# Performance work log

Hardware: AMD Instinct MI355X
Metric: run time of the kernel (lower is better)

## Reference

```python
import jax, jax.numpy as jnp
import numpy as np
import math

DIM = 1024
NH = 16
HD = DIM // NH
SEQ = 2048
B = 2
P = 16
HIDDEN = 2816  # multiple_of*ceil(int(2*4*dim/3)/multiple_of)


def justnorm(x, axis=-1):
    n = jnp.sqrt(jnp.sum(x * x, axis=axis, keepdims=True))
    return x / jnp.maximum(n, 1e-12)


def adafm_modulate(x, ftime, p):
    # x: [B,H,W]; ftime: [B, p*p] real
    Bb, H, W = x.shape
    xp = x.reshape(Bb, H // p, p, W // p, p).transpose(0, 1, 3, 2, 4).reshape(Bb, H // p, W // p, p * p)
    fspec = jnp.fft.fft2(xp)  # over last two axes (W//p, p*p)
    fspec = fspec * ftime.reshape(Bb, 1, 1, p * p)
    fout = jnp.fft.ifft2(fspec).real
    fout = fout.reshape(Bb, H // p, W // p, p, p).transpose(0, 1, 3, 2, 4).reshape(Bb, H, W)
    return fout


def apply_rotary(xq, xk, cos, sin):
    # xq,xk: [B,S,NH,HD]; cos,sin: [S, HD//2]
    def rot(t):
        tr = t.reshape(*t.shape[:-1], HD // 2, 2)
        a, b = tr[..., 0], tr[..., 1]
        c = cos[None, :, None, :]
        s = sin[None, :, None, :]
        ra = a * c - b * s
        rb = a * s + b * c
        return jnp.stack([ra, rb], axis=-1).reshape(t.shape)
    return rot(xq), rot(xk)


def attention(x, cos, sin, wq, wk, wv, wo, sqk):
    bsz, seqlen, _ = x.shape
    xq = (x @ wq).reshape(bsz, seqlen, NH, HD)
    xk = (x @ wk).reshape(bsz, seqlen, NH, HD)
    xv = (x @ wv).reshape(bsz, seqlen, NH, HD)
    xq, xk = apply_rotary(xq, xk, cos, sin)
    sqk_eff = (sqk * math.sqrt(DIM)).reshape(1, 1, NH, HD)  # sqk_init_value/sqk_init_scaling = sqrt(dim)
    xq = sqk_eff * justnorm(xq)
    xk = sqk_eff * justnorm(xk)
    scale = HD ** 0.5
    scores = jnp.einsum('bqhd,bkhd->bhqk', xq, xk) * scale
    attn = jax.nn.softmax(scores, axis=-1)
    out = jnp.einsum('bhqk,bkhd->bqhd', attn, xv).reshape(bsz, seqlen, DIM)
    return out @ wo


def feed_forward(x, w1, w2, w3, su, sv):
    x1 = x @ w1
    x3 = x @ w3
    scale = math.sqrt(HIDDEN)
    h = jax.nn.silu(x1 * sv * scale) * (x3 * su)
    return h @ w2


def setup_inputs() -> dict:
    key = jax.random.key(0)
    ks = jax.random.split(key, 12)
    inv = 1.0 / (10000.0 ** (np.arange(0, HD, 2, dtype=np.float32) / HD))
    ang = np.outer(np.arange(SEQ, dtype=np.float32), inv)
    s = 0.02
    return {
        'x': jax.random.normal(ks[0], (B, SEQ, DIM), jnp.float32),
        'freqs_cos': jnp.asarray(np.cos(ang), jnp.float32),
        'freqs_sin': jnp.asarray(np.sin(ang), jnp.float32),
        'adafm_input': jax.random.normal(ks[1], (B, DIM), jnp.float32),
        'wq': jax.random.normal(ks[2], (DIM, DIM), jnp.float32) * s,
        'wk': jax.random.normal(ks[3], (DIM, DIM), jnp.float32) * s,
        'wv': jax.random.normal(ks[4], (DIM, DIM), jnp.float32) * s,
        'wo': jax.random.normal(ks[5], (DIM, DIM), jnp.float32) * s,
        'sqk': jnp.full((DIM,), 1.0 / math.sqrt(DIM), jnp.float32),
        'w1': jax.random.normal(ks[6], (DIM, HIDDEN), jnp.float32) * s,
        'w2': jax.random.normal(ks[7], (HIDDEN, DIM), jnp.float32) * s,
        'w3': jax.random.normal(ks[8], (DIM, HIDDEN), jnp.float32) * s,
        'su': jnp.ones((HIDDEN,), jnp.float32),
        'sv': jnp.ones((HIDDEN,), jnp.float32),
        'proj_w': jax.random.normal(ks[9], (DIM, 2 * P * P), jnp.float32) * s,
        'proj_b': jnp.zeros((2 * P * P,), jnp.float32),
        'attn_alpha': jnp.full((DIM,), 0.05 / math.sqrt(DIM), jnp.float32),
        'mlp_alpha': jnp.full((DIM,), 0.05 / math.sqrt(DIM), jnp.float32),
    }


def reference(x, freqs_cos, freqs_sin, adafm_input, wq, wk, wv, wo, sqk, w1, w2, w3, su, sv, proj_w, proj_b, attn_alpha, mlp_alpha):
    # AdaFM projection: SiLU -> Linear
    t = jax.nn.silu(adafm_input) @ proj_w + proj_b  # [B, 2*P*P]
    msa_time, mlp_time = t[:, :P * P], t[:, P * P:]

    alpha_scale = 0.05 * math.sqrt(DIM)  # attn_alpha_init_value / attn_alpha_init_scaling
    lr = jnp.abs(attn_alpha * alpha_scale)
    h = justnorm(x)
    h_a = attention(adafm_modulate(x, msa_time, P), freqs_cos, freqs_sin, wq, wk, wv, wo, sqk)
    h_a = justnorm(h_a)
    x = justnorm(h + lr * (h_a - h))

    lr = jnp.abs(mlp_alpha * alpha_scale)
    h = justnorm(x)
    h_m = feed_forward(adafm_modulate(x, mlp_time, P), w1, w2, w3, su, sv)
    h_m = justnorm(h_m)
    x = justnorm(h + lr * (h_m - h))
    return x
```

## Files before the change

### kernel.cpp

```cpp
#include <hip/hip_runtime.h>
#include <hip/hip_bf16.h>
#include <math.h>

#define SEQ    2048
#define DIMN   1024
#define NHEAD  16
#define HDIM   64
#define BATCH  2
#define ROWS   4096
#define HIDDEN 2816
#define FCHUNK 2048
#define QKVS   3072

typedef __attribute__((ext_vector_type(8))) short short8;
typedef __attribute__((ext_vector_type(4))) float f32x4;
typedef unsigned short ushort_t;
typedef __attribute__((address_space(1))) void gas_t;
typedef __attribute__((address_space(3))) void las_t;

__device__ __forceinline__ float bfbits(ushort_t u){ return __uint_as_float(((unsigned)u) << 16); }
__device__ __forceinline__ ushort_t f2bu(float f){
  __hip_bfloat16 h = __float2bfloat16(f);
  return *reinterpret_cast<ushort_t*>(&h);
}
__device__ __forceinline__ ushort_t f2bu_t(float f){ return (ushort_t)(__float_as_uint(f) >> 16); }
__device__ __forceinline__ float ldv(const float* p){ return *p; }
__device__ __forceinline__ float ldv(const ushort_t* p){ return bfbits(*p); }
__device__ __forceinline__ void stv(float* p, float v){ *p = v; }
__device__ __forceinline__ void stv(ushort_t* p, float v){ *p = f2bu(v); }
__device__ __forceinline__ void async_cp16(const ushort_t* g, ushort_t* l){
  __builtin_amdgcn_global_load_lds((gas_t*)g, (las_t*)l, 16, 0, 0);
}
__device__ __forceinline__ ushort4 ld4u(const float* p){
  float4 v = *(const float4*)p;
  ushort4 u; u.x = f2bu(v.x); u.y = f2bu(v.y); u.z = f2bu(v.z); u.w = f2bu(v.w);
  return u;
}
__device__ __forceinline__ ushort4 ld4u(const ushort_t* p){ return *(const ushort4*)p; }

__global__ void k_time(const float* __restrict__ ada, const float* __restrict__ pw,
                       const float* __restrict__ pb, float* __restrict__ t){
  int b = blockIdx.x >> 9, o = blockIdx.x & 511, lane = threadIdx.x;
  float acc = 0.f;
  for(int i = lane; i < DIMN; i += 64){
    float a = ada[b*DIMN + i];
    float s = a / (1.f + expf(-a));
    acc += s * pw[i*512 + o];
  }
  for(int off = 32; off; off >>= 1) acc += __shfl_down(acc, off);
  if(lane == 0) t[b*512 + o] = acc + pb[o];
}

__global__ void k_gp(const float* __restrict__ t, ushort_t* __restrict__ Gpk){
  __shared__ float gl[256];
  int wb = blockIdx.x, kc = blockIdx.y, tid = threadIdx.x;
  int b = wb & 1, which = wb >> 1;
  const float C = 6.283185307179586f / 256.f;
  float acc = 0.f;
  for(int k = 0; k < 256; k++){
    float f = t[b*512 + which*256 + k];
    acc += f * cosf(C * (float)((k*tid) & 255));
  }
  gl[tid] = acc * (1.f/256.f);
  __syncthreads();
  ushort_t* ob = Gpk + ((size_t)(wb*8 + kc))*8192;
  for(int rep = 0; rep < 4; rep++){
    int n = rep*64 + (tid >> 2), mmb = (tid & 3)*8;
    short8 o;
    #pragma unroll
    for(int j = 0; j < 8; j++)
      o[j] = (short)f2bu(gl[(n - kc*32 - (mmb + j)) & 255]);
    *(short8*)(ob + n*32 + mmb) = o;
  }
}

#define APAD 264
#define GPAD 40
template<typename IN>
__global__ __launch_bounds__(256) void k_modmf(const IN* __restrict__ src,
        const ushort_t* __restrict__ Gpk, ushort_t* __restrict__ dst){
  __shared__ __align__(16) ushort_t Ap[64*APAD];
  __shared__ __align__(16) ushort_t Gs[128*GPAD];
  int nh = blockIdx.x, i = blockIdx.y, b = blockIdx.z;
  int tid = threadIdx.x, lane = tid & 63, w = tid >> 6;
  int l15 = lane & 15, quad = lane >> 4;
  const IN* xb = src + (size_t)b*SEQ*DIMN + (size_t)(i*16)*DIMN;
  int j = tid >> 2, c = (tid & 3)*4;
  #pragma unroll 4
  for(int rep = 0; rep < 16; rep++){
    ushort4 v4 = ld4u(xb + (size_t)rep*DIMN + tid*4);
    *(ushort4*)&Ap[j*APAD + rep*16 + c] = v4;
  }
  f32x4 acc[8];
  #pragma unroll
  for(int nt = 0; nt < 8; nt++){ acc[nt][0]=0.f; acc[nt][1]=0.f; acc[nt][2]=0.f; acc[nt][3]=0.f; }
  for(int kc = 0; kc < 8; kc++){
    __syncthreads();
    {
      const ushort_t* gsrc = Gpk + ((size_t)(b*8 + kc))*8192 + nh*4096;
      #pragma unroll
      for(int r2 = 0; r2 < 2; r2++){
        int n = r2*64 + (tid >> 2), mm = (tid & 3)*8;
        *(short8*)&Gs[n*GPAD + mm] = *(const short8*)(gsrc + r2*2048 + tid*8);
      }
    }
    __syncthreads();
    short8 af = *(const short8*)&Ap[(w*16 + l15)*APAD + kc*32 + quad*8];
    #pragma unroll
    for(int nt = 0; nt < 8; nt++){
      short8 bf = *(const short8*)&Gs[(nt*16 + l15)*GPAD + quad*8];
      acc[nt] = __builtin_amdgcn_mfma_f32_16x16x32_bf16(af, bf, acc[nt], 0, 0, 0);
    }
  }
  size_t ob = (size_t)b*SEQ*DIMN + (size_t)(i*16 + nh*8)*DIMN + (w*16 + quad*4)*16 + l15;
  #pragma unroll
  for(int nt = 0; nt < 8; nt++)
    #pragma unroll
    for(int t = 0; t < 4; t++)
      dst[ob + (size_t)nt*DIMN + t*16] = f2bu(acc[nt][t]);
}

__global__ void k_wt(const float* __restrict__ W, ushort_t* __restrict__ Wt, int K, int N){
  __shared__ float tile[32][33];
  int k0 = blockIdx.y*32, n0 = blockIdx.x*32;
  int r = threadIdx.x >> 3, c4 = (threadIdx.x & 7)*4;
  float4 v = *(const float4*)(W + (size_t)(k0 + r)*N + n0 + c4);
  tile[r][c4+0] = v.x; tile[r][c4+1] = v.y; tile[r][c4+2] = v.z; tile[r][c4+3] = v.w;
  __syncthreads();
  ushort4 o;
  o.x = f2bu(tile[c4+0][r]); o.y = f2bu(tile[c4+1][r]);
  o.z = f2bu(tile[c4+2][r]); o.w = f2bu(tile[c4+3][r]);
  *(ushort4*)(Wt + (size_t)(n0 + r)*K + k0 + c4) = o;
}

template<int BM, int BN, typename OUT>
__global__ __launch_bounds__(256) void k_gemm_mf(const ushort_t* __restrict__ A,
        const ushort_t* __restrict__ Wt, OUT* __restrict__ C, int N, int K){
  constexpr int MT = BM/32, NT = BN/32;
  constexpr int AI = BM/64, BI = BN/64;
  __shared__ __align__(16) ushort_t As[BM*32];
  __shared__ __align__(16) ushort_t Bs[BN*32];
  int tid = threadIdx.x, lane = tid & 63, w = tid >> 6;
  int l15 = lane & 15, quad = lane >> 4;
  int m0 = blockIdx.y*BM, n0 = blockIdx.x*BN;
  int wr = (w>>1)*(BM/2), wc = (w&1)*(BN/2);
  int srow = lane >> 2, scol = (lane & 3)*8;
  const ushort_t* ag[AI]; ushort_t* al[AI];
  const ushort_t* bg[BI]; ushort_t* bl[BI];
  #pragma unroll
  for(int i = 0; i < AI; i++){
    int rb = w*AI + i;
    ag[i] = A + (size_t)(m0 + rb*16 + srow)*K + scol;
    al[i] = As + rb*512 + lane*8;
  }
  #pragma unroll
  for(int i = 0; i < BI; i++){
    int rb = w*BI + i;
    bg[i] = Wt + (size_t)(n0 + rb*16 + srow)*K + scol;
    bl[i] = Bs + rb*512 + lane*8;
  }
  f32x4 acc[MT][NT];
  #pragma unroll
  for(int mt = 0; mt < MT; mt++)
    #pragma unroll
    for(int nt = 0; nt < NT; nt++)
      for(int t = 0; t < 4; t++) acc[mt][nt][t] = 0.f;
  for(int kk = 0; kk < K; kk += 32){
    __syncthreads();
    #pragma unroll
    for(int i = 0; i < AI; i++) async_cp16(ag[i] + kk, al[i]);
    #pragma unroll
    for(int i = 0; i < BI; i++) async_cp16(bg[i] + kk, bl[i]);
    __syncthreads();
    short8 af[MT], bf[NT];
    #pragma unroll
    for(int mt = 0; mt < MT; mt++) af[mt] = *(const short8*)&As[(wr + mt*16 + l15)*32 + quad*8];
    #pragma unroll
    for(int nt = 0; nt < NT; nt++) bf[nt] = *(const short8*)&Bs[(wc + nt*16 + l15)*32 + quad*8];
    #pragma unroll
    for(int mt = 0; mt < MT; mt++)
      #pragma unroll
      for(int nt = 0; nt < NT; nt++)
        acc[mt][nt] = __builtin_amdgcn_mfma_f32_16x16x32_bf16(af[mt], bf[nt], acc[mt][nt], 0, 0, 0);
  }
  #pragma unroll
  for(int mt = 0; mt < MT; mt++)
    #pragma unroll
    for(int nt = 0; nt < NT; nt++)
      #pragma unroll
      for(int t = 0; t < 4; t++)
        stv(C + (size_t)(m0 + wr + mt*16 + quad*4 + t)*N + n0 + wc + nt*16 + l15, acc[mt][nt][t]);
}

__global__ __launch_bounds__(256) void k_ffn12(const ushort_t* __restrict__ A,
        const ushort_t* __restrict__ W1t, const ushort_t* __restrict__ W3t,
        const float* __restrict__ su, const float* __restrict__ sv,
        ushort_t* __restrict__ H, int K){
  __shared__ __align__(16) ushort_t As[128*32];
  __shared__ __align__(16) ushort_t B1s[64*32];
  __shared__ __align__(16) ushort_t B3s[64*32];
  int tid = threadIdx.x, lane = tid & 63, w = tid >> 6;
  int l15 = lane & 15, quad = lane >> 4;
  int m0 = blockIdx.y*128, n0 = blockIdx.x*64;
  int wr = (w>>1)*64, wc = (w&1)*32;
  int srow = lane >> 2, scol = (lane & 3)*8;
  const ushort_t* ag[2]; ushort_t* al[2];
  #pragma unroll
  for(int i = 0; i < 2; i++){
    int rb = w*2 + i;
    ag[i] = A + (size_t)(m0 + rb*16 + srow)*K + scol;
    al[i] = As + rb*512 + lane*8;
  }
  const ushort_t* b1g = W1t + (size_t)(n0 + w*16 + srow)*K + scol;
  const ushort_t* b3g = W3t + (size_t)(n0 + w*16 + srow)*K + scol;
  ushort_t* b1l = B1s + w*512 + lane*8;
  ushort_t* b3l = B3s + w*512 + lane*8;
  f32x4 acc1[4][2], acc3[4][2];
  #pragma unroll
  for(int mt = 0; mt < 4; mt++)
    #pragma unroll
    for(int nt = 0; nt < 2; nt++)
      for(int t = 0; t < 4; t++){ acc1[mt][nt][t] = 0.f; acc3[mt][nt][t] = 0.f; }
  for(int kk = 0; kk < K; kk += 32){
    __syncthreads();
    async_cp16(ag[0] + kk, al[0]);
    async_cp16(ag[1] + kk, al[1]);
    async_cp16(b1g + kk, b1l);
    async_cp16(b3g + kk, b3l);
    __syncthreads();
    short8 af[4], b1f[2], b3f[2];
    #pragma unroll
    for(int mt = 0; mt < 4; mt++) af[mt] = *(const short8*)&As[(wr + mt*16 + l15)*32 + quad*8];
    #pragma unroll
    for(int nt = 0; nt < 2; nt++){
      b1f[nt] = *(const short8*)&B1s[(wc + nt*16 + l15)*32 + quad*8];
      b3f[nt] = *(const short8*)&B3s[(wc + nt*16 + l15)*32 + quad*8];
    }
    #pragma unroll
    for(int mt = 0; mt < 4; mt++)
      #pragma unroll
      for(int nt = 0; nt < 2; nt++){
        acc1[mt][nt] = __builtin_amdgcn_mfma_f32_16x16x32_bf16(af[mt], b1f[nt], acc1[mt][nt], 0, 0, 0);
        acc3[mt][nt] = __builtin_amdgcn_mfma_f32_16x16x32_bf16(af[mt], b3f[nt], acc3[mt][nt], 0, 0, 0);
      }
  }
  #pragma unroll
  for(int nt = 0; nt < 2; nt++){
    int n = n0 + wc + nt*16 + l15;
    float svv = sv[n] * 53.06599665f, suv = su[n];
    #pragma unroll
    for(int mt = 0; mt < 4; mt++)
      #pragma unroll
      for(int t = 0; t < 4; t++){
        float hpre = acc1[mt][nt][t] * svv;
        float sil = hpre / (1.f + expf(-hpre));
        float hv = sil * (acc3[mt][nt][t] * suv);
        H[(size_t)(m0 + wr + mt*16 + quad*4 + t)*HIDDEN + n] = f2bu(hv);
      }
  }
}

__global__ void k_qkvprep(ushort_t* __restrict__ qkv, const float* __restrict__ fc,
        const float* __restrict__ fs, const float* __restrict__ sqk){
  int w = threadIdx.x >> 6, d = threadIdx.x & 63;
  int h = blockIdx.x*4 + w, s = blockIdx.y, b = blockIdx.z;
  size_t ib = ((size_t)(b*SEQ + s))*QKVS + h*HDIM + d;
  float q = bfbits(qkv[ib]), k = bfbits(qkv[ib + 1024]);
  float qn = __shfl_xor(q, 1), kn = __shfl_xor(k, 1);
  int p = d >> 1;
  float c = fc[s*32 + p], sn = fs[s*32 + p];
  float qr, kr;
  if((d & 1) == 0){ qr = q*c - qn*sn; kr = k*c - kn*sn; }
  else            { qr = qn*sn + q*c; kr = kn*sn + k*c; }
  float sq = qr*qr, sk = kr*kr;
  for(int off = 32; off; off >>= 1){ sq += __shfl_xor(sq, off); sk += __shfl_xor(sk, off); }
  float scl = sqk[h*HDIM + d] * 32.f;
  qkv[ib]        = f2bu(scl * qr / fmaxf(sqrtf(sq), 1e-12f));
  qkv[ib + 1024] = f2bu(scl * kr / fmaxf(sqrtf(sk), 1e-12f));
}

__global__ void k_vt(const ushort_t* __restrict__ qkv, ushort_t* __restrict__ vto){
  __shared__ ushort_t tile[64][72];
  int s0 = blockIdx.x*64, h = blockIdx.y, b = blockIdx.z;
  int r = threadIdx.x >> 2, c = (threadIdx.x & 3)*16;
  const ushort_t* src = qkv + (size_t)(b*SEQ + s0 + r)*QKVS + 2048 + h*HDIM + c;
  *(short8*)&tile[r][c]     = *(const short8*)src;
  *(short8*)&tile[r][c + 8] = *(const short8*)(src + 8);
  __syncthreads();
  ushort_t* dst = vto + ((size_t)(b*NHEAD + h)*HDIM + r)*SEQ + s0 + c;
  for(int j = 0; j < 16; j += 4){
    ushort4 o;
    o.x = tile[c+j][r]; o.y = tile[c+j+1][r]; o.z = tile[c+j+2][r]; o.w = tile[c+j+3][r];
    *(ushort4*)(dst + j) = o;
  }
}

#define LSTR 72
__global__ __launch_bounds__(256) void k_flash_mf(const ushort_t* __restrict__ qkv,
        const ushort_t* __restrict__ vt, ushort_t* __restrict__ out){
  int qb = blockIdx.x, h = blockIdx.y, b = blockIdx.z;
  int tid = threadIdx.x, lane = tid & 63, w = tid >> 6;
  int l15 = lane & 15, quad = lane >> 4;
  __shared__ __align__(16) ushort_t Ks[64*LSTR], Vts[64*LSTR];
  __shared__ __align__(16) ushort_t Ps[4][32*LSTR];
  size_t qkb = (size_t)b*SEQ*QKVS + h*HDIM;
  const ushort_t* vb = vt + (size_t)(b*NHEAD + h)*HDIM*SEQ;
  short8 qf[2][2];
  #pragma unroll
  for(int qm = 0; qm < 2; qm++){
    const ushort_t* qrow = qkv + qkb + (size_t)(qb*128 + w*32 + qm*16 + l15)*QKVS;
    qf[qm][0] = *(const short8*)(qrow + quad*8);
    qf[qm][1] = *(const short8*)(qrow + 32 + quad*8);
  }
  f32x4 o_acc[2][4];
  #pragma unroll
  for(int qm = 0; qm < 2; qm++)
    #pragma unroll
    for(int g = 0; g < 4; g++){ o_acc[qm][g][0]=0.f; o_acc[qm][g][1]=0.f; o_acc[qm][g][2]=0.f; o_acc[qm][g][3]=0.f; }
  float lsum[2] = {0.f, 0.f};
  int sr = tid >> 2, sc = tid & 3;
  const float C1 = 11.54156036f;
  const float C2 = 11.90223409f;
  for(int ch = 0; ch < SEQ/64; ch++){
    __syncthreads();
    {
      const ushort_t* krow = qkv + qkb + (size_t)(b ? 0 : 0) + (size_t)(ch*64 + sr)*QKVS + 1024 + sc*16;
      short8 k0 = *(const short8*)krow, k1 = *(const short8*)(krow + 8);
      const ushort_t* vrow = vb + (size_t)sr*SEQ + ch*64 + sc*16;
      short8 v0 = *(const short8*)vrow, v1 = *(const short8*)(vrow + 8);
      *(short8*)&Ks[sr*LSTR + sc*16]      = k0;
      *(short8*)&Ks[sr*LSTR + sc*16 + 8]  = k1;
      *(short8*)&Vts[sr*LSTR + sc*16]     = v0;
      *(short8*)&Vts[sr*LSTR + sc*16 + 8] = v1;
    }
    __syncthreads();
    #pragma unroll
    for(int g = 0; g < 4; g++){
      short8 k0 = *(const short8*)&Ks[(g*16 + l15)*LSTR + quad*8];
      short8 k1 = *(const short8*)&Ks[(g*16 + l15)*LSTR + 32 + quad*8];
      #pragma unroll
      for(int qm = 0; qm < 2; qm++){
        f32x4 sa; sa[0]=0.f; sa[1]=0.f; sa[2]=0.f; sa[3]=0.f;
        sa = __builtin_amdgcn_mfma_f32_16x16x32_bf16(k0, qf[qm][0], sa, 0, 0, 0);
        sa = __builtin_amdgcn_mfma_f32_16x16x32_bf16(k1, qf[qm][1], sa, 0, 0, 0);
        float e0 = exp2f(fmaf(sa[0], C1, -C2));
        float e1 = exp2f(fmaf(sa[1], C1, -C2));
        float e2 = exp2f(fmaf(sa[2], C1, -C2));
        float e3 = exp2f(fmaf(sa[3], C1, -C2));
        lsum[qm] += (e0 + e1) + (e2 + e3);
        ushort4 pk;
        pk.x = f2bu_t(e0); pk.y = f2bu_t(e1); pk.z = f2bu_t(e2); pk.w = f2bu_t(e3);
        *(ushort4*)&Ps[w][(qm*16 + l15)*LSTR + g*16 + quad*4] = pk;
      }
    }
    __syncthreads();
    short8 a[2][2];
    #pragma unroll
    for(int qm = 0; qm < 2; qm++){
      a[qm][0] = *(const short8*)&Ps[w][(qm*16 + l15)*LSTR + quad*8];
      a[qm][1] = *(const short8*)&Ps[w][(qm*16 + l15)*LSTR + 32 + quad*8];
    }
    #pragma unroll
    for(int g = 0; g < 4; g++){
      short8 b0 = *(const short8*)&Vts[(g*16 + l15)*LSTR + quad*8];
      short8 b1 = *(const short8*)&Vts[(g*16 + l15)*LSTR + 32 + quad*8];
      #pragma unroll
      for(int qm = 0; qm < 2; qm++){
        o_acc[qm][g] = __builtin_amdgcn_mfma_f32_16x16x32_bf16(a[qm][0], b0, o_acc[qm][g], 0, 0, 0);
        o_acc[qm][g] = __builtin_amdgcn_mfma_f32_16x16x32_bf16(a[qm][1], b1, o_acc[qm][g], 0, 0, 0);
      }
    }
  }
  #pragma unroll
  for(int qm = 0; qm < 2; qm++){
    float ls = lsum[qm];
    ls += __shfl_xor(ls, 16);
    ls += __shfl_xor(ls, 32);
    #pragma unroll
    for(int t = 0; t < 4; t++){
      float inv = 1.f / __shfl(ls, quad*4 + t);
      #pragma unroll
      for(int g = 0; g < 4; g++)
        out[(size_t)b*SEQ*DIMN + (size_t)(qb*128 + w*32 + qm*16 + quad*4 + t)*DIMN + h*HDIM + g*16 + l15]
          = f2bu(o_acc[qm][g][t] * inv);
    }
  }
}

__device__ __forceinline__ float blockReduceSum(float v, float* red){
  for(int off = 32; off; off >>= 1) v += __shfl_xor(v, off);
  int wid = threadIdx.x >> 6;
  if((threadIdx.x & 63) == 0) red[wid] = v;
  __syncthreads();
  float tot = red[0] + red[1] + red[2] + red[3];
  __syncthreads();
  return tot;
}

template<typename T1, typename T2, typename TO>
__global__ void k_rn(const T1* __restrict__ x, const T2* __restrict__ ha,
        const float* __restrict__ alpha, TO* __restrict__ xo){
  __shared__ float red[4];
  int row = blockIdx.x, tid = threadIdx.x;
  size_t base = (size_t)row * DIMN;
  float xs[4], hs[4], cs[4];
  float s1 = 0.f, s2 = 0.f;
  for(int j = 0; j < 4; j++){
    int i = tid + j*256;
    float xv = ldv(x + base + i);  xs[j] = xv; s1 += xv*xv;
    float hv = ldv(ha + base + i); hs[j] = hv; s2 += hv*hv;
  }
  s1 = blockReduceSum(s1, red);
  s2 = blockReduceSum(s2, red);
  float r1 = 1.f / fmaxf(sqrtf(s1), 1e-12f);
  float r2 = 1.f / fmaxf(sqrtf(s2), 1e-12f);
  float s3 = 0.f;
  for(int j = 0; j < 4; j++){
    int i = tid + j*256;
    float lr = fabsf(alpha[i] * 1.6f);
    float hn = xs[j] * r1;
    float cv = hn + lr*(hs[j]*r2 - hn);
    cs[j] = cv; s3 += cv*cv;
  }
  s3 = blockReduceSum(s3, red);
  float r3 = 1.f / fmaxf(sqrtf(s3), 1e-12f);
  for(int j = 0; j < 4; j++){
    int i = tid + j*256;
    stv(xo + base + i, cs[j] * r3);
  }
}

extern "C" void kernel_launch(void* const* d_in, const int* in_sizes, int n_in,
                              void* d_out, int out_size, void* d_ws, size_t ws_size,
                              hipStream_t stream){
  const float* x   = (const float*)d_in[0];
  const float* fc  = (const float*)d_in[1];
  const float* fs  = (const float*)d_in[2];
  const float* ada = (const float*)d_in[3];
  const float* wq  = (const float*)d_in[4];
  const float* wk  = (const float*)d_in[5];
  const float* wv  = (const float*)d_in[6];
  const float* wo  = (const float*)d_in[7];
  const float* sqk = (const float*)d_in[8];
  const float* w1  = (const float*)d_in[9];
  const float* w2  = (const float*)d_in[10];
  const float* w3  = (const float*)d_in[11];
  const float* su  = (const float*)d_in[12];
  const float* sv  = (const float*)d_in[13];
  const float* pw  = (const float*)d_in[14];
  const float* pb  = (const float*)d_in[15];
  const float* aal = (const float*)d_in[16];
  const float* mal = (const float*)d_in[17];
  float* out = (float*)d_out;

  const size_t MM = (size_t)DIMN*DIMN;
  const size_t HM = (size_t)HIDDEN*DIMN;
  const size_t F  = (size_t)ROWS*DIMN;
  char* wsb = (char*)d_ws;
  float* t = (float*)wsb;
  ushort_t* Gpk = (ushort_t*)(wsb + 16384);
  ushort_t* wqT = Gpk + 262144;
  ushort_t* wkT = wqT + MM;
  ushort_t* wvT = wkT + MM;
  ushort_t* woT = wvT + MM;
  ushort_t* w1T = woT + MM;
  ushort_t* w3T = w1T + HM;
  ushort_t* w2T = w3T + HM;
  ushort_t* P1  = w2T + HM;
  ushort_t* QKV = P1 + F;
  ushort_t* Ha  = QKV;
  ushort_t* M2  = QKV + F;
  ushort_t* Hm  = QKV + 2*F;
  ushort_t* a1  = QKV + 3*F;
  ushort_t* Vt  = a1;

  dim3 blk(256);

  k_time<<<dim3(1024), dim3(64), 0, stream>>>(ada, pw, pb, t);
  k_gp<<<dim3(4,8), blk, 0, stream>>>(t, Gpk);

  k_wt<<<dim3(32,32), blk, 0, stream>>>(wq, wqT, DIMN, DIMN);
  k_wt<<<dim3(32,32), blk, 0, stream>>>(wk, wkT, DIMN, DIMN);
  k_wt<<<dim3(32,32), blk, 0, stream>>>(wv, wvT, DIMN, DIMN);
  k_wt<<<dim3(32,32), blk, 0, stream>>>(wo, woT, DIMN, DIMN);
  k_wt<<<dim3(HIDDEN/32,32), blk, 0, stream>>>(w1, w1T, DIMN, HIDDEN);
  k_wt<<<dim3(HIDDEN/32,32), blk, 0, stream>>>(w3, w3T, DIMN, HIDDEN);
  k_wt<<<dim3(32,HIDDEN/32), blk, 0, stream>>>(w2, w2T, HIDDEN, DIMN);

  k_modmf<float><<<dim3(2,128,BATCH), blk, 0, stream>>>(x, Gpk, P1);
  k_gemm_mf<128,128,ushort_t><<<dim3(24,32), blk, 0, stream>>>(P1, wqT, QKV, QKVS, DIMN);
  k_qkvprep<<<dim3(NHEAD/4,SEQ,BATCH), blk, 0, stream>>>(QKV, fc, fs, sqk);
  k_vt<<<dim3(SEQ/64,NHEAD,BATCH), blk, 0, stream>>>(QKV, Vt);
  k_flash_mf<<<dim3(SEQ/128,NHEAD,BATCH), blk, 0, stream>>>(QKV, Vt, P1);
  k_gemm_mf<128,128,ushort_t><<<dim3(8,32), blk, 0, stream>>>(P1, woT, Ha, DIMN, DIMN);
  k_rn<float,ushort_t,ushort_t><<<dim3(ROWS), blk, 0, stream>>>(x, Ha, aal, P1);

  k_modmf<ushort_t><<<dim3(2,128,BATCH), blk, 0, stream>>>(P1, Gpk + 131072, M2);
  for(int c2 = 0; c2 < ROWS/FCHUNK; c2++){
    const ushort_t* Ac = M2 + (size_t)c2*FCHUNK*DIMN;
    k_ffn12<<<dim3(HIDDEN/64,FCHUNK/128), blk, 0, stream>>>(Ac, w1T, w3T, su, sv, a1, DIMN);
    k_gemm_mf<128,128,ushort_t><<<dim3(8,FCHUNK/128), blk, 0, stream>>>(a1, w2T, Hm + (size_t)c2*FCHUNK*DIMN, DIMN, HIDDEN);
  }

  k_rn<ushort_t,ushort_t,float><<<dim3(ROWS), blk, 0, stream>>>(P1, Hm, mal, out);
}
```

Measured before the change: 578.5 us.

## Halve flash query tile, prefetch K/V into registers, shrink output GEMM tiles

The flash attention kernel now handles 64 queries per block (16 per wave) instead of 128. This doubles the grid and cuts registers and LDS per block. K/V tiles for the next chunk are loaded into registers while the current chunk is computed, and the barrier between writing and reading P is dropped because each wave only touches its own P slice. The wo and w2 GEMM launches switch to smaller tiles so more blocks fill the GPU, at the cost of less reuse per block and more redundant K/V loads across blocks.

After: 512.4 us. 11.4% less time.

```diff
diff --git a/kernel.cpp b/kernel.cpp
--- a/kernel.cpp
+++ b/kernel.cpp
@@ -302,88 +302,74 @@
   int tid = threadIdx.x, lane = tid & 63, w = tid >> 6;
   int l15 = lane & 15, quad = lane >> 4;
   __shared__ __align__(16) ushort_t Ks[64*LSTR], Vts[64*LSTR];
-  __shared__ __align__(16) ushort_t Ps[4][32*LSTR];
+  __shared__ __align__(16) ushort_t Ps[4][16*LSTR];
   size_t qkb = (size_t)b*SEQ*QKVS + h*HDIM;
+  size_t ob  = (size_t)b*SEQ*DIMN + h*HDIM;
   const ushort_t* vb = vt + (size_t)(b*NHEAD + h)*HDIM*SEQ;
-  short8 qf[2][2];
-  #pragma unroll
-  for(int qm = 0; qm < 2; qm++){
-    const ushort_t* qrow = qkv + qkb + (size_t)(qb*128 + w*32 + qm*16 + l15)*QKVS;
-    qf[qm][0] = *(const short8*)(qrow + quad*8);
-    qf[qm][1] = *(const short8*)(qrow + 32 + quad*8);
-  }
-  f32x4 o_acc[2][4];
-  #pragma unroll
-  for(int qm = 0; qm < 2; qm++)
-    #pragma unroll
-    for(int g = 0; g < 4; g++){ o_acc[qm][g][0]=0.f; o_acc[qm][g][1]=0.f; o_acc[qm][g][2]=0.f; o_acc[qm][g][3]=0.f; }
-  float lsum[2] = {0.f, 0.f};
+  short8 qf0, qf1;
+  {
+    const ushort_t* qrow = qkv + qkb + (size_t)(qb*64 + w*16 + l15)*QKVS;
+    qf0 = *(const short8*)(qrow + quad*8);
+    qf1 = *(const short8*)(qrow + 32 + quad*8);
+  }
+  f32x4 o_acc[4];
+  #pragma unroll
+  for(int g = 0; g < 4; g++){ o_acc[g][0]=0.f; o_acc[g][1]=0.f; o_acc[g][2]=0.f; o_acc[g][3]=0.f; }
+  float lsum = 0.f;
   int sr = tid >> 2, sc = tid & 3;
+  const ushort_t* kbase = qkv + qkb + 1024 + (size_t)sr*QKVS + sc*16;
+  const ushort_t* vbase = vb + (size_t)sr*SEQ + sc*16;
+  short8 kr0 = *(const short8*)kbase,       kr1 = *(const short8*)(kbase + 8);
+  short8 vr0 = *(const short8*)vbase,       vr1 = *(const short8*)(vbase + 8);
   const float C1 = 11.54156036f;
   const float C2 = 11.90223409f;
   for(int ch = 0; ch < SEQ/64; ch++){
     __syncthreads();
-    {
-      const ushort_t* krow = qkv + qkb + (size_t)(b ? 0 : 0) + (size_t)(ch*64 + sr)*QKVS + 1024 + sc*16;
-      short8 k0 = *(const short8*)krow, k1 = *(const short8*)(krow + 8);
-      const ushort_t* vrow = vb + (size_t)sr*SEQ + ch*64 + sc*16;
-      short8 v0 = *(const short8*)vrow, v1 = *(const short8*)(vrow + 8);
-      *(short8*)&Ks[sr*LSTR + sc*16]      = k0;
-      *(short8*)&Ks[sr*LSTR + sc*16 + 8]  = k1;
-      *(short8*)&Vts[sr*LSTR + sc*16]     = v0;
-      *(short8*)&Vts[sr*LSTR + sc*16 + 8] = v1;
+    *(short8*)&Ks[sr*LSTR + sc*16]      = kr0;
+    *(short8*)&Ks[sr*LSTR + sc*16 + 8]  = kr1;
+    *(short8*)&Vts[sr*LSTR + sc*16]     = vr0;
+    *(short8*)&Vts[sr*LSTR + sc*16 + 8] = vr1;
+    if(ch + 1 < SEQ/64){
+      const ushort_t* kn = kbase + (size_t)(ch + 1)*64*QKVS;
+      const ushort_t* vn = vbase + (ch + 1)*64;
+      kr0 = *(const short8*)kn; kr1 = *(const short8*)(kn + 8);
+      vr0 = *(const short8*)vn; vr1 = *(const short8*)(vn + 8);
     }
     __syncthreads();
     #pragma unroll
     for(int g = 0; g < 4; g++){
+      f32x4 sa; sa[0]=0.f; sa[1]=0.f; sa[2]=0.f; sa[3]=0.f;
       short8 k0 = *(const short8*)&Ks[(g*16 + l15)*LSTR + quad*8];
       short8 k1 = *(const short8*)&Ks[(g*16 + l15)*LSTR + 32 + quad*8];
-      #pragma unroll
-      for(int qm = 0; qm < 2; qm++){
-        f32x4 sa; sa[0]=0.f; sa[1]=0.f; sa[2]=0.f; sa[3]=0.f;
-        sa = __builtin_amdgcn_mfma_f32_16x16x32_bf16(k0, qf[qm][0], sa, 0, 0, 0);
-        sa = __builtin_amdgcn_mfma_f32_16x16x32_bf16(k1, qf[qm][1], sa, 0, 0, 0);
-        float e0 = exp2f(fmaf(sa[0], C1, -C2));
-        float e1 = exp2f(fmaf(sa[1], C1, -C2));
-        float e2 = exp2f(fmaf(sa[2], C1, -C2));
-        float e3 = exp2f(fmaf(sa[3], C1, -C2));
-        lsum[qm] += (e0 + e1) + (e2 + e3);
-        ushort4 pk;
-        pk.x = f2bu_t(e0); pk.y = f2bu_t(e1); pk.z = f2bu_t(e2); pk.w = f2bu_t(e3);
-        *(ushort4*)&Ps[w][(qm*16 + l15)*LSTR + g*16 + quad*4] = pk;
-      }
-    }
-    __syncthreads();
-    short8 a[2][2];
-    #pragma unroll
-    for(int qm = 0; qm < 2; qm++){
-      a[qm][0] = *(const short8*)&Ps[w][(qm*16 + l15)*LSTR + quad*8];
-      a[qm][1] = *(const short8*)&Ps[w][(qm*16 + l15)*LSTR + 32 + quad*8];
-    }
+      sa = __builtin_amdgcn_mfma_f32_16x16x32_bf16(k0, qf0, sa, 0, 0, 0);
+      sa = __builtin_amdgcn_mfma_f32_16x16x32_bf16(k1, qf1, sa, 0, 0, 0);
+      float e0 = exp2f(fmaf(sa[0], C1, -C2));
+      float e1 = exp2f(fmaf(sa[1], C1, -C2));
+      float e2 = exp2f(fmaf(sa[2], C1, -C2));
+      float e3 = exp2f(fmaf(sa[3], C1, -C2));
+      lsum += (e0 + e1) + (e2 + e3);
+      ushort4 pk;
+      pk.x = f2bu_t(e0); pk.y = f2bu_t(e1); pk.z = f2bu_t(e2); pk.w = f2bu_t(e3);
+      *(ushort4*)&Ps[w][l15*LSTR + g*16 + quad*4] = pk;
+    }
+    short8 a0 = *(const short8*)&Ps[w][l15*LSTR + quad*8];
+    short8 a1 = *(const short8*)&Ps[w][l15*LSTR + 32 + quad*8];
     #pragma unroll
     for(int g = 0; g < 4; g++){
       short8 b0 = *(const short8*)&Vts[(g*16 + l15)*LSTR + quad*8];
       short8 b1 = *(const short8*)&Vts[(g*16 + l15)*LSTR + 32 + quad*8];
-      #pragma unroll
-      for(int qm = 0; qm < 2; qm++){
-        o_acc[qm][g] = __builtin_amdgcn_mfma_f32_16x16x32_bf16(a[qm][0], b0, o_acc[qm][g], 0, 0, 0);
-        o_acc[qm][g] = __builtin_amdgcn_mfma_f32_16x16x32_bf16(a[qm][1], b1, o_acc[qm][g], 0, 0, 0);
-      }
-    }
-  }
-  #pragma unroll
-  for(int qm = 0; qm < 2; qm++){
-    float ls = lsum[qm];
-    ls += __shfl_xor(ls, 16);
-    ls += __shfl_xor(ls, 32);
-    #pragma unroll
-    for(int t = 0; t < 4; t++){
-      float inv = 1.f / __shfl(ls, quad*4 + t);
-      #pragma unroll
-      for(int g = 0; g < 4; g++)
-        out[(size_t)b*SEQ*DIMN + (size_t)(qb*128 + w*32 + qm*16 + quad*4 + t)*DIMN + h*HDIM + g*16 + l15]
-          = f2bu(o_acc[qm][g][t] * inv);
-    }
+      o_acc[g] = __builtin_amdgcn_mfma_f32_16x16x32_bf16(a0, b0, o_acc[g], 0, 0, 0);
+      o_acc[g] = __builtin_amdgcn_mfma_f32_16x16x32_bf16(a1, b1, o_acc[g], 0, 0, 0);
+    }
+  }
+  lsum += __shfl_xor(lsum, 16);
+  lsum += __shfl_xor(lsum, 32);
+  #pragma unroll
+  for(int t = 0; t < 4; t++){
+    float inv = 1.f / __shfl(lsum, quad*4 + t);
+    #pragma unroll
+    for(int g = 0; g < 4; g++)
+      out[ob + (size_t)(qb*64 + w*16 + quad*4 + t)*DIMN + g*16 + l15] = f2bu(o_acc[g][t] * inv);
   }
 }
 
@@ -491,15 +477,15 @@
   k_gemm_mf<128,128,ushort_t><<<dim3(24,32), blk, 0, stream>>>(P1, wqT, QKV, QKVS, DIMN);
   k_qkvprep<<<dim3(NHEAD/4,SEQ,BATCH), blk, 0, stream>>>(QKV, fc, fs, sqk);
   k_vt<<<dim3(SEQ/64,NHEAD,BATCH), blk, 0, stream>>>(QKV, Vt);
-  k_flash_mf<<<dim3(SEQ/128,NHEAD,BATCH), blk, 0, stream>>>(QKV, Vt, P1);
-  k_gemm_mf<128,128,ushort_t><<<dim3(8,32), blk, 0, stream>>>(P1, woT, Ha, DIMN, DIMN);
+  k_flash_mf<<<dim3(SEQ/64,NHEAD,BATCH), blk, 0, stream>>>(QKV, Vt, P1);
+  k_gemm_mf<128,64,ushort_t><<<dim3(16,32), blk, 0, stream>>>(P1, woT, Ha, DIMN, DIMN);
   k_rn<float,ushort_t,ushort_t><<<dim3(ROWS), blk, 0, stream>>>(x, Ha, aal, P1);
 
   k_modmf<ushort_t><<<dim3(2,128,BATCH), blk, 0, stream>>>(P1, Gpk + 131072, M2);
   for(int c2 = 0; c2 < ROWS/FCHUNK; c2++){
     const ushort_t* Ac = M2 + (size_t)c2*FCHUNK*DIMN;
     k_ffn12<<<dim3(HIDDEN/64,FCHUNK/128), blk, 0, stream>>>(Ac, w1T, w3T, su, sv, a1, DIMN);
-    k_gemm_mf<128,128,ushort_t><<<dim3(8,FCHUNK/128), blk, 0, stream>>>(a1, w2T, Hm + (size_t)c2*FCHUNK*DIMN, DIMN, HIDDEN);
+    k_gemm_mf<64,64,ushort_t><<<dim3(16,FCHUNK/64), blk, 0, stream>>>(a1, w2T, Hm + (size_t)c2*FCHUNK*DIMN, DIMN, HIDDEN);
   }
 
   k_rn<ushort_t,ushort_t,float><<<dim3(ROWS), blk, 0, stream>>>(P1, Hm, mal, out);
```
